# Performance work log

Hardware: AMD Instinct MI355X
Metric: run time of the kernel (lower is better)

The kernel has to match this reference:

```python
import jax, jax.numpy as jnp
import numpy as np
import math

B, N, T, F_IN, F_OUT = 4, 512, 128, 64, 64


def setup_inputs() -> dict:
    key = jax.random.key(0)
    k1, k2, k3 = jax.random.split(key, 3)
    x = jax.random.normal(k1, (B, N, T, F_IN), dtype=jnp.float32)
    adj = jax.random.uniform(k2, (N, N), dtype=jnp.float32)
    theta_w = jax.random.normal(k3, (F_OUT, F_IN), dtype=jnp.float32) * (1.0 / math.sqrt(F_IN))
    return {"x": x, "sym_norm_Adj_matrix": adj, "Theta_w": theta_w}


def reference(x, sym_norm_Adj_matrix, Theta_w):
    b, n, t, f_in = x.shape
    inv_sqrt_f = 1.0 / math.sqrt(f_in)
    # (B, N, T, F) -> (B*T, N, F)
    xt = jnp.transpose(x, (0, 2, 1, 3)).reshape(b * t, n, f_in)
    # attention scores per (batch*time): (BT, N, N)
    score = jnp.einsum('gnf,gmf->gnm', xt, xt) * inv_sqrt_f
    score = jax.nn.softmax(score, axis=-1) * inv_sqrt_f  # second /sqrt(F_in) in forward
    # post-softmax multiplicative adjacency masking, then graph conv matmul
    masked = sym_norm_Adj_matrix[None, :, :] * score      # (BT, N, N)
    agg = jnp.einsum('gnm,gmf->gnf', masked, xt)          # (BT, N, F_in)
    out = jax.nn.relu(agg @ Theta_w.T)                    # (BT, N, F_out)
    # (B, T, N, F_out) -> (B, N, T, F_out)
    return jnp.transpose(out.reshape(b, t, n, -1), (0, 2, 1, 3))
```

## Files before the change

kernel.cpp:

```cpp
#include <hip/hip_runtime.h>
#include <math.h>

#define B_   4
#define N_   512
#define T_   128
#define F_   64
#define QB   128
#define NSTR (T_*F_)
#define KT_  32
#define TILE 4096
#define ATILE 16384
#define FTILE 8192

typedef __attribute__((ext_vector_type(8))) short  s8v;
typedef __attribute__((ext_vector_type(4))) float  f4v;

union F8 { s8v v; unsigned u[4]; uint2 u2[2]; };

__device__ __forceinline__ unsigned cvt_pk(float lo, float hi) {
    unsigned r;
    asm("v_cvt_pk_bf16_f32 %0, %1, %2" : "=v"(r) : "v"(lo), "v"(hi));
    return r;
}

template<int OFF>
__device__ __forceinline__ uint2 tr16(unsigned a) {
    uint2 d;
    asm volatile("ds_read_b64_tr_b16 %0, %1 offset:%2" : "=v"(d) : "v"(a), "i"(OFF));
    return d;
}

__device__ __forceinline__ void gload16(const void* g, void* l) {
    __builtin_amdgcn_global_load_lds(
        (const __attribute__((address_space(1))) void*)g,
        (__attribute__((address_space(3))) void*)l, 16, 0, 0);
}

#define EXPK 0.18033688f

__global__ __launch_bounds__(256)
void xpose_kernel(const float* __restrict__ x, unsigned short* __restrict__ xt)
{
    __shared__ char lds[32*1024];

    const int tid = threadIdx.x;
    const int lane = tid & 63;
    const int w    = tid >> 6;
    const int n0 = blockIdx.x * 8;
    const int t0 = blockIdx.y * 32;
    const int b  = blockIdx.z;

    const int tA = tid >> 3;
    const int f0 = (tid & 7) * 8;

    #pragma unroll
    for (int np = 0; np < 8; ++np) {
        const float* gp = x + ((size_t)(b*N_ + n0 + np)*T_ + t0 + tA)*F_ + f0;
        float4 a = *(const float4*)gp;
        float4 c = *(const float4*)(gp + 4);
        uint4 u;
        u.x = cvt_pk(a.x, a.y); u.y = cvt_pk(a.z, a.w);
        u.z = cvt_pk(c.x, c.y); u.w = cvt_pk(c.z, c.w);
        *(uint4*)(lds + tA*1024 + np*128 + ((f0*2) ^ ((tA & 7) << 4))) = u;
    }
    __syncthreads();

    #pragma unroll
    for (int p = 0; p < 8; ++p) {
        int t  = p*4 + w;
        int np = lane >> 3;
        int i  = lane & 7;
        uint4 u = *(const uint4*)(lds + t*1024 + np*128 + ((i*16) ^ ((t & 7) << 4)));
        *(uint4*)(xt + ((size_t)(b*T_ + t0 + t)*N_ + n0 + np)*F_ + i*8) = u;
    }
}

__global__ __launch_bounds__(512, 4)
void sgcn_1bar_kernel(const unsigned short* __restrict__ xt,
                      const float* __restrict__ adj,
                      const float* __restrict__ theta,
                      float* __restrict__ out)
{
    __shared__ char lds[16384 + 2*ATILE];

    const int tid  = threadIdx.x;
    const int lane = tid & 63;
    const int w    = tid >> 6;
    const int s    = w >> 2;
    const int wq   = w & 3;
    const int c15  = lane & 15;
    const int g4   = lane >> 4;

    const int bid = blockIdx.x;
    const int qx  = bid & 3;
    const int tp  = bid >> 2;
    const int g   = 2*tp + s;
    const int b   = g >> 7;
    const int t   = g & 127;
    const int qb  = qx*QB;
    const int q0  = qb + 32*wq;

    const unsigned short* xtg = xt + (size_t)g*N_*F_;
    char* Kbase = lds + s*(2*TILE);
    char* Abase = lds + 16384;

    const int ksoff = (((lane>>3)*4 + ((lane&7)>>1)))*F_ + wq*16 + (lane&1)*8;

    int aoff[2];
    #pragma unroll
    for (int i = 0; i < 2; ++i) {
        int r = i*64 + w*8 + (lane >> 3);
        aoff[i] = (qb + r)*N_ + 4*((lane & 7) ^ (r & 7));
    }

    auto stageK = [&](int kt1) {
        gload16(xtg + (size_t)kt1*KT_*F_ + ksoff, Kbase + (kt1 & 1)*TILE + wq*1024);
    };
    auto stageA = [&](int kt1) {
        char* ab = Abase + (kt1 & 1)*ATILE;
        #pragma unroll
        for (int i = 0; i < 2; ++i)
            gload16(adj + aoff[i] + kt1*KT_, ab + i*8192 + w*1024);
    };

    stageK(0);
    stageA(0);

    F8 qf[2][2];
    #pragma unroll
    for (int qt = 0; qt < 2; ++qt)
      #pragma unroll
      for (int kk = 0; kk < 2; ++kk)
        qf[qt][kk].v = *(const s8v*)(xtg + (size_t)(q0 + 16*qt + c15)*F_ + 32*kk + 8*g4);

    f4v  Oacc[4][2];
    float l_acc[2] = {0.f, 0.f};
    #pragma unroll
    for (int ft = 0; ft < 4; ++ft)
      #pragma unroll
      for (int qt = 0; qt < 2; ++qt) Oacc[ft][qt] = (f4v)0.f;

    const int afoff = (g4>>1)*1024 + (c15>>2)*128 + (c15&3)*32 + (g4&1)*16;

    for (int kt = 0; kt < 16; ++kt) {
        __syncthreads();

        const char* bufC  = Kbase + (size_t)(kt & 1)*TILE;
        const char* abufC = Abase + (size_t)(kt & 1)*ATILE;
        if (kt < 15) { stageK(kt+1); stageA(kt+1); }

        F8 pb[2];
        #pragma unroll
        for (int mt = 0; mt < 2; ++mt) {
            F8 af0, af1;
            af0.v = *(const s8v*)(bufC + afoff + mt*512);
            af1.v = *(const s8v*)(bufC + afoff + mt*512 + 2048);

            #pragma unroll
            for (int qt = 0; qt < 2; ++qt) {
                const int r = 32*wq + 16*qt + c15;
                float4 av = *(const float4*)(abufC + r*128 + ((((mt<<2)+g4) ^ (r & 7)) << 4));
                f4v sv = (f4v)0.f;
                __builtin_amdgcn_s_setprio(1);
                sv = __builtin_amdgcn_mfma_f32_16x16x32_bf16(af0.v, qf[qt][0].v, sv, 0, 0, 0);
                sv = __builtin_amdgcn_mfma_f32_16x16x32_bf16(af1.v, qf[qt][1].v, sv, 0, 0, 0);
                __builtin_amdgcn_s_setprio(0);
                float e0 = __builtin_amdgcn_exp2f(sv[0] * EXPK);
                float e1 = __builtin_amdgcn_exp2f(sv[1] * EXPK);
                float e2 = __builtin_amdgcn_exp2f(sv[2] * EXPK);
                float e3 = __builtin_amdgcn_exp2f(sv[3] * EXPK);
                l_acc[qt] += (e0 + e1) + (e2 + e3);
                pb[qt].u[2*mt  ] = cvt_pk(e0*av.x, e1*av.y);
                pb[qt].u[2*mt+1] = cvt_pk(e2*av.z, e3*av.w);
            }
        }

        const unsigned va = (unsigned)(uintptr_t)bufC + (unsigned)(lane * 8);
        {
            F8 vf0, vf1, vf2, vf3;
            vf0.u2[0] = tr16<   0>(va); vf0.u2[1] = tr16< 512>(va);
            vf1.u2[0] = tr16<1024>(va); vf1.u2[1] = tr16<1536>(va);
            vf2.u2[0] = tr16<2048>(va); vf2.u2[1] = tr16<2560>(va);
            vf3.u2[0] = tr16<3072>(va); vf3.u2[1] = tr16<3584>(va);
            asm volatile("s_waitcnt lgkmcnt(0)" ::: "memory");
            __builtin_amdgcn_sched_barrier(0);
            __builtin_amdgcn_s_setprio(1);
            #pragma unroll
            for (int qt = 0; qt < 2; ++qt) {
                Oacc[0][qt] = __builtin_amdgcn_mfma_f32_16x16x32_bf16(vf0.v, pb[qt].v, Oacc[0][qt], 0, 0, 0);
                Oacc[1][qt] = __builtin_amdgcn_mfma_f32_16x16x32_bf16(vf1.v, pb[qt].v, Oacc[1][qt], 0, 0, 0);
                Oacc[2][qt] = __builtin_amdgcn_mfma_f32_16x16x32_bf16(vf2.v, pb[qt].v, Oacc[2][qt], 0, 0, 0);
                Oacc[3][qt] = __builtin_amdgcn_mfma_f32_16x16x32_bf16(vf3.v, pb[qt].v, Oacc[3][qt], 0, 0, 0);
            }
            __builtin_amdgcn_s_setprio(0);
        }
    }

    float inv[2];
    #pragma unroll
    for (int qt = 0; qt < 2; ++qt) {
        float lv = l_acc[qt];
        lv += __shfl_xor(lv, 16);
        lv += __shfl_xor(lv, 32);
        inv[qt] = 0.125f / lv;
    }

    F8 ob[2][2];
    #pragma unroll
    for (int qt = 0; qt < 2; ++qt)
      #pragma unroll
      for (int kk = 0; kk < 2; ++kk) {
        f4v o0 = Oacc[2*kk][qt], o1 = Oacc[2*kk+1][qt];
        ob[qt][kk].u[0] = cvt_pk(o0[0]*inv[qt], o0[1]*inv[qt]);
        ob[qt][kk].u[1] = cvt_pk(o0[2]*inv[qt], o0[3]*inv[qt]);
        ob[qt][kk].u[2] = cvt_pk(o1[0]*inv[qt], o1[1]*inv[qt]);
        ob[qt][kk].u[3] = cvt_pk(o1[2]*inv[qt], o1[3]*inv[qt]);
      }

    F8 tf[4][2];
    #pragma unroll
    for (int ot = 0; ot < 4; ++ot)
      #pragma unroll
      for (int kk = 0; kk < 2; ++kk) {
        const float* tp2 = theta + (size_t)(16*ot + c15)*F_ + 32*kk + 4*g4;
        float4 a = *(const float4*)tp2;
        float4 c = *(const float4*)(tp2 + 16);
        tf[ot][kk].u[0] = cvt_pk(a.x, a.y);
        tf[ot][kk].u[1] = cvt_pk(a.z, a.w);
        tf[ot][kk].u[2] = cvt_pk(c.x, c.y);
        tf[ot][kk].u[3] = cvt_pk(c.z, c.w);
      }

    f4v R[4][2];
    #pragma unroll
    for (int ot = 0; ot < 4; ++ot)
      #pragma unroll
      for (int qt = 0; qt < 2; ++qt) R[ot][qt] = (f4v)0.f;

    #pragma unroll
    for (int kk = 0; kk < 2; ++kk)
      #pragma unroll
      for (int ot = 0; ot < 4; ++ot)
        #pragma unroll
        for (int qt = 0; qt < 2; ++qt)
          R[ot][qt] = __builtin_amdgcn_mfma_f32_16x16x32_bf16(tf[ot][kk].v, ob[qt][kk].v, R[ot][qt], 0, 0, 0);

    #pragma unroll
    for (int ot = 0; ot < 4; ++ot)
      #pragma unroll
      for (int qt = 0; qt < 2; ++qt) {
        float4 v;
        v.x = fmaxf(R[ot][qt][0], 0.f);
        v.y = fmaxf(R[ot][qt][1], 0.f);
        v.z = fmaxf(R[ot][qt][2], 0.f);
        v.w = fmaxf(R[ot][qt][3], 0.f);
        int q  = q0 + 16*qt + c15;
        int fo = 16*ot + 4*g4;
        *(float4*)(out + ((size_t)(b*N_ + q)*T_ + t)*F_ + fo) = v;
      }
}

__global__ __launch_bounds__(256, 3)
void sgcn_fb_kernel(const float* __restrict__ x,
                    const float* __restrict__ adj,
                    const float* __restrict__ theta,
                    float* __restrict__ out)
{
    __shared__ char ldsbuf[2*FTILE];

    const int tid  = threadIdx.x;
    const int lane = tid & 63;
    const int w    = tid >> 6;
    const int c15  = lane & 15;
    const int g4   = lane >> 4;

    const int g  = blockIdx.y;
    const int b  = g >> 7;
    const int t  = g & 127;
    const int q0 = blockIdx.x*QB + 32*w;

    const float* xg = x + (size_t)b*N_*NSTR + (size_t)t*F_;

    F8 qf[2][2];
    #pragma unroll
    for (int qt = 0; qt < 2; ++qt)
      #pragma unroll
      for (int kk = 0; kk < 2; ++kk) {
        const float* qp = xg + (size_t)(q0 + 16*qt + c15)*NSTR + 32*kk + 8*g4;
        float4 a = *(const float4*)qp;
        float4 c = *(const float4*)(qp + 4);
        qf[qt][kk].u[0] = cvt_pk(a.x, a.y);
        qf[qt][kk].u[1] = cvt_pk(a.z, a.w);
        qf[qt][kk].u[2] = cvt_pk(c.x, c.y);
        qf[qt][kk].u[3] = cvt_pk(c.z, c.w);
      }

    f4v  Oacc[4][2];
    float l_acc[2] = {0.f, 0.f};
    #pragma unroll
    for (int ft = 0; ft < 4; ++ft)
      #pragma unroll
      for (int qt = 0; qt < 2; ++qt) Oacc[ft][qt] = (f4v)0.f;

    const int nrow  = tid >> 4;
    const int stoff = (c15>>2)*2048 + w*128 + g4*32 + (c15&3)*8;
    const int afoff = (g4>>1)*2048 + (c15>>2)*128 + (c15&3)*32 + (g4&1)*16;

    const float* arow0 = adj + (size_t)(q0 +      c15)*N_ + 4*g4;
    const float* arow1 = adj + (size_t)(q0 + 16 + c15)*N_ + 4*g4;

    float4 xv[4];
    auto stage = [&](char* buf) {
        #pragma unroll
        for (int it = 0; it < 4; ++it) {
            unsigned p0 = cvt_pk(xv[it].x, xv[it].y);
            unsigned p1 = cvt_pk(xv[it].z, xv[it].w);
            *(uint2*)(buf + stoff + it*512) = make_uint2(p0, p1);
        }
    };
    auto loadK = [&](int k0) {
        #pragma unroll
        for (int it = 0; it < 4; ++it)
            xv[it] = *(const float4*)(xg + (size_t)(k0 + nrow + 16*it)*NSTR + 4*c15);
    };

    loadK(0);
    stage(ldsbuf);
    const unsigned xb = (unsigned)(uintptr_t)ldsbuf;

    for (int kt = 0; kt < 8; ++kt) {
        __syncthreads();
        char* bufC = ldsbuf + (size_t)(kt & 1) * FTILE;
        char* bufN = ldsbuf + (size_t)((kt & 1) ^ 1) * FTILE;
        if (kt < 7) loadK((kt+1)*64);

        F8 pb[2][2];
        #pragma unroll
        for (int mt = 0; mt < 4; ++mt) {
            float4 av0 = *(const float4*)(arow0 + kt*64 + 16*mt);
            float4 av1 = *(const float4*)(arow1 + kt*64 + 16*mt);
            F8 af0, af1;
            af0.v = *(const s8v*)(bufC + afoff + mt*512);
            af1.v = *(const s8v*)(bufC + afoff + mt*512 + 4096);
            #pragma unroll
            for (int qt = 0; qt < 2; ++qt) {
                f4v sv = (f4v)0.f;
                sv = __builtin_amdgcn_mfma_f32_16x16x32_bf16(af0.v, qf[qt][0].v, sv, 0, 0, 0);
                sv = __builtin_amdgcn_mfma_f32_16x16x32_bf16(af1.v, qf[qt][1].v, sv, 0, 0, 0);
                float e0 = __builtin_amdgcn_exp2f(sv[0] * EXPK);
                float e1 = __builtin_amdgcn_exp2f(sv[1] * EXPK);
                float e2 = __builtin_amdgcn_exp2f(sv[2] * EXPK);
                float e3 = __builtin_amdgcn_exp2f(sv[3] * EXPK);
                l_acc[qt] += (e0 + e1) + (e2 + e3);
                float4 av = qt ? av1 : av0;
                pb[qt][mt>>1].u[2*(mt&1)  ] = cvt_pk(e0*av.x, e1*av.y);
                pb[qt][mt>>1].u[2*(mt&1)+1] = cvt_pk(e2*av.z, e3*av.w);
            }
        }

        const unsigned va = xb + (unsigned)((kt & 1) * FTILE) + (unsigned)(lane * 8);
        {
            F8 vf0, vf1, vf2, vf3;
            vf0.u2[0] = tr16<   0>(va); vf0.u2[1] = tr16< 512>(va);
            vf1.u2[0] = tr16<2048>(va); vf1.u2[1] = tr16<2560>(va);
            vf2.u2[0] = tr16<4096>(va); vf2.u2[1] = tr16<4608>(va);
            vf3.u2[0] = tr16<6144>(va); vf3.u2[1] = tr16<6656>(va);
            asm volatile("s_waitcnt lgkmcnt(0)" ::: "memory");
            __builtin_amdgcn_sched_barrier(0);
            #pragma unroll
            for (int qt = 0; qt < 2; ++qt) {
                Oacc[0][qt] = __builtin_amdgcn_mfma_f32_16x16x32_bf16(vf0.v, pb[qt][0].v, Oacc[0][qt], 0, 0, 0);
                Oacc[1][qt] = __builtin_amdgcn_mfma_f32_16x16x32_bf16(vf1.v, pb[qt][0].v, Oacc[1][qt], 0, 0, 0);
                Oacc[2][qt] = __builtin_amdgcn_mfma_f32_16x16x32_bf16(vf2.v, pb[qt][0].v, Oacc[2][qt], 0, 0, 0);
                Oacc[3][qt] = __builtin_amdgcn_mfma_f32_16x16x32_bf16(vf3.v, pb[qt][0].v, Oacc[3][qt], 0, 0, 0);
            }
        }
        {
            F8 vf0, vf1, vf2, vf3;
            vf0.u2[0] = tr16<1024>(va); vf0.u2[1] = tr16<1536>(va);
            vf1.u2[0] = tr16<3072>(va); vf1.u2[1] = tr16<3584>(va);
            vf2.u2[0] = tr16<5120>(va); vf2.u2[1] = tr16<5632>(va);
            vf3.u2[0] = tr16<7168>(va); vf3.u2[1] = tr16<7680>(va);
            asm volatile("s_waitcnt lgkmcnt(0)" ::: "memory");
            __builtin_amdgcn_sched_barrier(0);
            #pragma unroll
            for (int qt = 0; qt < 2; ++qt) {
                Oacc[0][qt] = __builtin_amdgcn_mfma_f32_16x16x32_bf16(vf0.v, pb[qt][1].v, Oacc[0][qt], 0, 0, 0);
                Oacc[1][qt] = __builtin_amdgcn_mfma_f32_16x16x32_bf16(vf1.v, pb[qt][1].v, Oacc[1][qt], 0, 0, 0);
                Oacc[2][qt] = __builtin_amdgcn_mfma_f32_16x16x32_bf16(vf2.v, pb[qt][1].v, Oacc[2][qt], 0, 0, 0);
                Oacc[3][qt] = __builtin_amdgcn_mfma_f32_16x16x32_bf16(vf3.v, pb[qt][1].v, Oacc[3][qt], 0, 0, 0);
            }
        }
        if (kt < 7) stage(bufN);
    }

    float inv[2];
    #pragma unroll
    for (int qt = 0; qt < 2; ++qt) {
        float lv = l_acc[qt];
        lv += __shfl_xor(lv, 16);
        lv += __shfl_xor(lv, 32);
        inv[qt] = 0.125f / lv;
    }

    F8 ob[2][2];
    #pragma unroll
    for (int qt = 0; qt < 2; ++qt)
      #pragma unroll
      for (int kk = 0; kk < 2; ++kk) {
        f4v o0 = Oacc[2*kk][qt], o1 = Oacc[2*kk+1][qt];
        ob[qt][kk].u[0] = cvt_pk(o0[0]*inv[qt], o0[1]*inv[qt]);
        ob[qt][kk].u[1] = cvt_pk(o0[2]*inv[qt], o0[3]*inv[qt]);
        ob[qt][kk].u[2] = cvt_pk(o1[0]*inv[qt], o1[1]*inv[qt]);
        ob[qt][kk].u[3] = cvt_pk(o1[2]*inv[qt], o1[3]*inv[qt]);
      }

    F8 tf[4][2];
    #pragma unroll
    for (int ot = 0; ot < 4; ++ot)
      #pragma unroll
      for (int kk = 0; kk < 2; ++kk) {
        const float* tp2 = theta + (size_t)(16*ot + c15)*F_ + 32*kk + 4*g4;
        float4 a = *(const float4*)tp2;
        float4 c = *(const float4*)(tp2 + 16);
        tf[ot][kk].u[0] = cvt_pk(a.x, a.y);
        tf[ot][kk].u[1] = cvt_pk(a.z, a.w);
        tf[ot][kk].u[2] = cvt_pk(c.x, c.y);
        tf[ot][kk].u[3] = cvt_pk(c.z, c.w);
      }

    f4v R[4][2];
    #pragma unroll
    for (int ot = 0; ot < 4; ++ot)
      #pragma unroll
      for (int qt = 0; qt < 2; ++qt) R[ot][qt] = (f4v)0.f;

    #pragma unroll
    for (int kk = 0; kk < 2; ++kk)
      #pragma unroll
      for (int ot = 0; ot < 4; ++ot)
        #pragma unroll
        for (int qt = 0; qt < 2; ++qt)
          R[ot][qt] = __builtin_amdgcn_mfma_f32_16x16x32_bf16(tf[ot][kk].v, ob[qt][kk].v, R[ot][qt], 0, 0, 0);

    #pragma unroll
    for (int ot = 0; ot < 4; ++ot)
      #pragma unroll
      for (int qt = 0; qt < 2; ++qt) {
        float4 v;
        v.x = fmaxf(R[ot][qt][0], 0.f);
        v.y = fmaxf(R[ot][qt][1], 0.f);
        v.z = fmaxf(R[ot][qt][2], 0.f);
        v.w = fmaxf(R[ot][qt][3], 0.f);
        int q  = q0 + 16*qt + c15;
        int fo = 16*ot + 4*g4;
        *(float4*)(out + ((size_t)(b*N_ + q)*T_ + t)*F_ + fo) = v;
      }
}

extern "C" void kernel_launch(void* const* d_in, const int* in_sizes, int n_in,
                              void* d_out, int out_size, void* d_ws, size_t ws_size,
                              hipStream_t stream) {
    const float* x     = (const float*)d_in[0];
    const float* adj   = (const float*)d_in[1];
    const float* theta = (const float*)d_in[2];
    float* out = (float*)d_out;

    const size_t need = (size_t)B_*T_*N_*F_*2;
    if (ws_size >= need) {
        unsigned short* xt = (unsigned short*)d_ws;
        xpose_kernel<<<dim3(N_/8, T_/32, B_), 256, 0, stream>>>(x, xt);
        sgcn_1bar_kernel<<<1024, 512, 0, stream>>>(xt, adj, theta, out);
    } else {
        dim3 grid(N_ / QB, B_ * T_);
        sgcn_fb_kernel<<<grid, 256, 0, stream>>>(x, adj, theta, out);
    }
}
```

Before: 91.27 us.

## Halve block size so each wave handles 64 query rows instead of 32

The main kernel now runs 256 threads per block, and each wave covers 64 query rows (four 16-row tiles), so every K/V and adjacency fragment loaded from LDS feeds twice as many MFMAs. Staging is spread over fewer threads with more loads each. The k-loop is manually unrolled by two with fixed buffer parity, the s_setprio hints are dropped, and the theta projection is computed one output tile at a time to cap register use. Doubling the accumulators raises register pressure, and occupancy falls from 4 to 3 blocks, which may hurt latency hiding.

```diff
diff --git a/kernel.cpp b/kernel.cpp
--- a/kernel.cpp
+++ b/kernel.cpp
@@ -75,19 +75,19 @@
     }
 }
 
-__global__ __launch_bounds__(512, 4)
-void sgcn_1bar_kernel(const unsigned short* __restrict__ xt,
-                      const float* __restrict__ adj,
-                      const float* __restrict__ theta,
-                      float* __restrict__ out)
+__global__ __launch_bounds__(256, 3)
+void sgcn_q64_kernel(const unsigned short* __restrict__ xt,
+                     const float* __restrict__ adj,
+                     const float* __restrict__ theta,
+                     float* __restrict__ out)
 {
     __shared__ char lds[16384 + 2*ATILE];
 
     const int tid  = threadIdx.x;
     const int lane = tid & 63;
     const int w    = tid >> 6;
-    const int s    = w >> 2;
-    const int wq   = w & 3;
+    const int s    = w >> 1;
+    const int wwq  = w & 1;
     const int c15  = lane & 15;
     const int g4   = lane >> 4;
 
@@ -98,58 +98,64 @@
     const int b   = g >> 7;
     const int t   = g & 127;
     const int qb  = qx*QB;
-    const int q0  = qb + 32*wq;
+    const int q0  = qb + 64*wwq;
 
     const unsigned short* xtg = xt + (size_t)g*N_*F_;
     char* Kbase = lds + s*(2*TILE);
     char* Abase = lds + 16384;
 
-    const int ksoff = (((lane>>3)*4 + ((lane&7)>>1)))*F_ + wq*16 + (lane&1)*8;
-
-    int aoff[2];
-    #pragma unroll
-    for (int i = 0; i < 2; ++i) {
-        int r = i*64 + w*8 + (lane >> 3);
-        aoff[i] = (qb + r)*N_ + 4*((lane & 7) ^ (r & 7));
-    }
-
-    auto stageK = [&](int kt1) {
-        gload16(xtg + (size_t)kt1*KT_*F_ + ksoff, Kbase + (kt1 & 1)*TILE + wq*1024);
-    };
-    auto stageA = [&](int kt1) {
-        char* ab = Abase + (kt1 & 1)*ATILE;
-        #pragma unroll
-        for (int i = 0; i < 2; ++i)
-            gload16(adj + aoff[i] + kt1*KT_, ab + i*8192 + w*1024);
-    };
-
-    stageK(0);
-    stageA(0);
-
-    F8 qf[2][2];
-    #pragma unroll
-    for (int qt = 0; qt < 2; ++qt)
+    int ksoff[2];
+    #pragma unroll
+    for (int i = 0; i < 2; ++i)
+        ksoff[i] = ((lane>>3)*4 + ((lane&7)>>1))*F_ + (2*wwq + i)*16 + (lane&1)*8;
+
+    int aoff[4];
+    #pragma unroll
+    for (int i = 0; i < 4; ++i)
+        aoff[i] = (qb + 32*i + 8*w + (lane>>3))*N_ + 4*((lane&7) ^ (lane>>3));
+
+    #pragma unroll
+    for (int i = 0; i < 2; ++i)
+        gload16(xtg + ksoff[i], Kbase + (2*wwq + i)*1024);
+    #pragma unroll
+    for (int i = 0; i < 4; ++i)
+        gload16(adj + aoff[i], Abase + i*4096 + w*1024);
+
+    F8 qf[4][2];
+    #pragma unroll
+    for (int qt = 0; qt < 4; ++qt)
       #pragma unroll
       for (int kk = 0; kk < 2; ++kk)
         qf[qt][kk].v = *(const s8v*)(xtg + (size_t)(q0 + 16*qt + c15)*F_ + 32*kk + 8*g4);
 
-    f4v  Oacc[4][2];
-    float l_acc[2] = {0.f, 0.f};
+    f4v  Oacc[4][4];
+    float l_acc[4] = {0.f, 0.f, 0.f, 0.f};
     #pragma unroll
     for (int ft = 0; ft < 4; ++ft)
       #pragma unroll
-      for (int qt = 0; qt < 2; ++qt) Oacc[ft][qt] = (f4v)0.f;
+      for (int qt = 0; qt < 4; ++qt) Oacc[ft][qt] = (f4v)0.f;
 
     const int afoff = (g4>>1)*1024 + (c15>>2)*128 + (c15&3)*32 + (g4&1)*16;
-
-    for (int kt = 0; kt < 16; ++kt) {
+    const int arow  = 64*wwq + c15;
+    const unsigned kvab = (unsigned)(uintptr_t)Kbase + (unsigned)(lane * 8);
+
+    auto body = [&](int kt, int p) {
         __syncthreads();
 
-        const char* bufC  = Kbase + (size_t)(kt & 1)*TILE;
-        const char* abufC = Abase + (size_t)(kt & 1)*ATILE;
-        if (kt < 15) { stageK(kt+1); stageA(kt+1); }
-
-        F8 pb[2];
+        const char* bufC  = Kbase + p*TILE;
+        const char* abufC = Abase + p*ATILE;
+        if (kt < 15) {
+            const unsigned short* sb = xtg + (size_t)(kt+1)*KT_*F_;
+            #pragma unroll
+            for (int i = 0; i < 2; ++i)
+                gload16(sb + ksoff[i], Kbase + (p^1)*TILE + (2*wwq + i)*1024);
+            const float* ab = adj + (kt+1)*KT_;
+            #pragma unroll
+            for (int i = 0; i < 4; ++i)
+                gload16(ab + aoff[i], Abase + (p^1)*ATILE + i*4096 + w*1024);
+        }
+
+        F8 pb[4];
         #pragma unroll
         for (int mt = 0; mt < 2; ++mt) {
             F8 af0, af1;
@@ -157,14 +163,12 @@
             af1.v = *(const s8v*)(bufC + afoff + mt*512 + 2048);
 
             #pragma unroll
-            for (int qt = 0; qt < 2; ++qt) {
-                const int r = 32*wq + 16*qt + c15;
+            for (int qt = 0; qt < 4; ++qt) {
+                const int r = arow + 16*qt;
                 float4 av = *(const float4*)(abufC + r*128 + ((((mt<<2)+g4) ^ (r & 7)) << 4));
                 f4v sv = (f4v)0.f;
-                __builtin_amdgcn_s_setprio(1);
                 sv = __builtin_amdgcn_mfma_f32_16x16x32_bf16(af0.v, qf[qt][0].v, sv, 0, 0, 0);
                 sv = __builtin_amdgcn_mfma_f32_16x16x32_bf16(af1.v, qf[qt][1].v, sv, 0, 0, 0);
-                __builtin_amdgcn_s_setprio(0);
                 float e0 = __builtin_amdgcn_exp2f(sv[0] * EXPK);
                 float e1 = __builtin_amdgcn_exp2f(sv[1] * EXPK);
                 float e2 = __builtin_amdgcn_exp2f(sv[2] * EXPK);
@@ -175,39 +179,40 @@
             }
         }
 
-        const unsigned va = (unsigned)(uintptr_t)bufC + (unsigned)(lane * 8);
-        {
-            F8 vf0, vf1, vf2, vf3;
-            vf0.u2[0] = tr16<   0>(va); vf0.u2[1] = tr16< 512>(va);
-            vf1.u2[0] = tr16<1024>(va); vf1.u2[1] = tr16<1536>(va);
-            vf2.u2[0] = tr16<2048>(va); vf2.u2[1] = tr16<2560>(va);
-            vf3.u2[0] = tr16<3072>(va); vf3.u2[1] = tr16<3584>(va);
-            asm volatile("s_waitcnt lgkmcnt(0)" ::: "memory");
-            __builtin_amdgcn_sched_barrier(0);
-            __builtin_amdgcn_s_setprio(1);
-            #pragma unroll
-            for (int qt = 0; qt < 2; ++qt) {
-                Oacc[0][qt] = __builtin_amdgcn_mfma_f32_16x16x32_bf16(vf0.v, pb[qt].v, Oacc[0][qt], 0, 0, 0);
-                Oacc[1][qt] = __builtin_amdgcn_mfma_f32_16x16x32_bf16(vf1.v, pb[qt].v, Oacc[1][qt], 0, 0, 0);
-                Oacc[2][qt] = __builtin_amdgcn_mfma_f32_16x16x32_bf16(vf2.v, pb[qt].v, Oacc[2][qt], 0, 0, 0);
-                Oacc[3][qt] = __builtin_amdgcn_mfma_f32_16x16x32_bf16(vf3.v, pb[qt].v, Oacc[3][qt], 0, 0, 0);
-            }
-            __builtin_amdgcn_s_setprio(0);
-        }
-    }
-
-    float inv[2];
-    #pragma unroll
-    for (int qt = 0; qt < 2; ++qt) {
+        const unsigned va = kvab + (unsigned)(p*TILE);
+        F8 vf0, vf1, vf2, vf3;
+        vf0.u2[0] = tr16<   0>(va); vf0.u2[1] = tr16< 512>(va);
+        vf1.u2[0] = tr16<1024>(va); vf1.u2[1] = tr16<1536>(va);
+        vf2.u2[0] = tr16<2048>(va); vf2.u2[1] = tr16<2560>(va);
+        vf3.u2[0] = tr16<3072>(va); vf3.u2[1] = tr16<3584>(va);
+        asm volatile("s_waitcnt lgkmcnt(0)" ::: "memory");
+        __builtin_amdgcn_sched_barrier(0);
+        #pragma unroll
+        for (int qt = 0; qt < 4; ++qt) {
+            Oacc[0][qt] = __builtin_amdgcn_mfma_f32_16x16x32_bf16(vf0.v, pb[qt].v, Oacc[0][qt], 0, 0, 0);
+            Oacc[1][qt] = __builtin_amdgcn_mfma_f32_16x16x32_bf16(vf1.v, pb[qt].v, Oacc[1][qt], 0, 0, 0);
+            Oacc[2][qt] = __builtin_amdgcn_mfma_f32_16x16x32_bf16(vf2.v, pb[qt].v, Oacc[2][qt], 0, 0, 0);
+            Oacc[3][qt] = __builtin_amdgcn_mfma_f32_16x16x32_bf16(vf3.v, pb[qt].v, Oacc[3][qt], 0, 0, 0);
+        }
+    };
+
+    for (int kt = 0; kt < 16; kt += 2) {
+        body(kt,     0);
+        body(kt + 1, 1);
+    }
+
+    float inv[4];
+    #pragma unroll
+    for (int qt = 0; qt < 4; ++qt) {
         float lv = l_acc[qt];
         lv += __shfl_xor(lv, 16);
         lv += __shfl_xor(lv, 32);
         inv[qt] = 0.125f / lv;
     }
 
-    F8 ob[2][2];
-    #pragma unroll
-    for (int qt = 0; qt < 2; ++qt)
+    F8 ob[4][2];
+    #pragma unroll
+    for (int qt = 0; qt < 4; ++qt)
       #pragma unroll
       for (int kk = 0; kk < 2; ++kk) {
         f4v o0 = Oacc[2*kk][qt], o1 = Oacc[2*kk+1][qt];
@@ -231,33 +236,29 @@
         tf[ot][kk].u[3] = cvt_pk(c.z, c.w);
       }
 
-    f4v R[4][2];
-    #pragma unroll
-    for (int ot = 0; ot < 4; ++ot)
-      #pragma unroll
-      for (int qt = 0; qt < 2; ++qt) R[ot][qt] = (f4v)0.f;
-
-    #pragma unroll
-    for (int kk = 0; kk < 2; ++kk)
-      #pragma unroll
-      for (int ot = 0; ot < 4; ++ot)
-        #pragma unroll
-        for (int qt = 0; qt < 2; ++qt)
-          R[ot][qt] = __builtin_amdgcn_mfma_f32_16x16x32_bf16(tf[ot][kk].v, ob[qt][kk].v, R[ot][qt], 0, 0, 0);
-
-    #pragma unroll
-    for (int ot = 0; ot < 4; ++ot)
-      #pragma unroll
-      for (int qt = 0; qt < 2; ++qt) {
-        float4 v;
-        v.x = fmaxf(R[ot][qt][0], 0.f);
-        v.y = fmaxf(R[ot][qt][1], 0.f);
-        v.z = fmaxf(R[ot][qt][2], 0.f);
-        v.w = fmaxf(R[ot][qt][3], 0.f);
-        int q  = q0 + 16*qt + c15;
-        int fo = 16*ot + 4*g4;
-        *(float4*)(out + ((size_t)(b*N_ + q)*T_ + t)*F_ + fo) = v;
-      }
+    #pragma unroll
+    for (int ot = 0; ot < 4; ++ot) {
+        f4v R[4];
+        #pragma unroll
+        for (int qt = 0; qt < 4; ++qt) R[qt] = (f4v)0.f;
+        #pragma unroll
+        for (int kk = 0; kk < 2; ++kk)
+          #pragma unroll
+          for (int qt = 0; qt < 4; ++qt)
+            R[qt] = __builtin_amdgcn_mfma_f32_16x16x32_bf16(tf[ot][kk].v, ob[qt][kk].v, R[qt], 0, 0, 0);
+
+        #pragma unroll
+        for (int qt = 0; qt < 4; ++qt) {
+            float4 v;
+            v.x = fmaxf(R[qt][0], 0.f);
+            v.y = fmaxf(R[qt][1], 0.f);
+            v.z = fmaxf(R[qt][2], 0.f);
+            v.w = fmaxf(R[qt][3], 0.f);
+            int q  = q0 + 16*qt + c15;
+            int fo = 16*ot + 4*g4;
+            *(float4*)(out + ((size_t)(b*N_ + q)*T_ + t)*F_ + fo) = v;
+        }
+    }
 }
 
 __global__ __launch_bounds__(256, 3)
@@ -470,7 +471,7 @@
     if (ws_size >= need) {
         unsigned short* xt = (unsigned short*)d_ws;
         xpose_kernel<<<dim3(N_/8, T_/32, B_), 256, 0, stream>>>(x, xt);
-        sgcn_1bar_kernel<<<1024, 512, 0, stream>>>(xt, adj, theta, out);
+        sgcn_q64_kernel<<<1024, 256, 0, stream>>>(xt, adj, theta, out);
     } else {
         dim3 grid(N_ / QB, B_ * T_);
         sgcn_fb_kernel<<<grid, 256, 0, stream>>>(x, adj, theta, out);
```

After: 201.2 us. 2.2x slower.
